# Kernel optimization log

Hardware: AMD Instinct MI355X
Metric: run time of the kernel (lower is better)

Reference implementation:

```python
import jax, jax.numpy as jnp
import numpy as np

N = 50000      # nodes
E = 800000     # edges
F_IN = 512     # num_features
H = 128        # hidden


def setup_inputs() -> dict:
    key = jax.random.key(0)
    ks = jax.random.split(key, 10)
    edge_index = jax.random.randint(ks[0], (2, E), 0, N, dtype=jnp.int64 if jax.config.jax_enable_x64 else jnp.int32)
    x = jax.random.normal(ks[1], (N, F_IN), jnp.float32)
    weights = jax.random.uniform(ks[2], (E,), jnp.float32)
    def w(i, shape, fan):
        return jax.random.normal(ks[i], shape, jnp.float32) / np.sqrt(fan).astype(np.float32)
    return {
        "edge_index": edge_index,
        "x": x,
        "weights": weights,
        "W_lin1": w(3, (F_IN, H), F_IN), "b_lin1": jnp.zeros((H,), jnp.float32),
        "W_conv1": w(4, (H, 2 * H), H), "b_conv1": jnp.zeros((2 * H,), jnp.float32),
        "W_mu": w(5, (2 * H, H), 2 * H), "b_mu": jnp.zeros((H,), jnp.float32),
        "W_lin": w(6, (2 * H, 1), 2 * H), "b_lin": jnp.zeros((1,), jnp.float32),
    }


def gcn_conv(x, W, b, src, dst, ew, n):
    """PyG GCNConv with edge weights: add self-loops (weight 1), symmetric norm, scatter-add."""
    loop = jnp.arange(n, dtype=src.dtype)
    s2 = jnp.concatenate([src, loop])
    d2 = jnp.concatenate([dst, loop])
    w2 = jnp.concatenate([ew, jnp.ones((n,), x.dtype)])
    deg = jax.ops.segment_sum(w2, d2, num_segments=n)          # weighted in-degree incl. self-loop
    dinv = jnp.where(deg > 0, deg, 1.0) ** -0.5
    dinv = jnp.where(deg > 0, dinv, 0.0)
    norm = dinv[s2] * w2 * dinv[d2]                            # [E+N]
    h = x @ W                                                   # [N, out]
    out = jax.ops.segment_sum(h[s2] * norm[:, None], d2, num_segments=n)
    return out + b


def reference(edge_index, x, weights, W_lin1, b_lin1, W_conv1, b_conv1, W_mu, b_mu, W_lin, b_lin):
    n = x.shape[0]
    src, dst = edge_index[0], edge_index[1]
    # eval mode: dropout is identity, VGAE.encode returns mu
    h = x @ W_lin1 + b_lin1                                     # lin1
    h = jax.nn.relu(gcn_conv(h, W_conv1, b_conv1, src, dst, weights, n))
    z = gcn_conv(h, W_mu, b_mu, src, dst, weights, n)           # mu == embeddings
    emb_edges = jnp.concatenate([z[src], z[dst]], axis=1)       # [E, 2H]
    out = jax.nn.sigmoid(emb_edges @ W_lin + b_lin)
    return out.squeeze(-1)                                      # [E]
```

## Files before the change

kernel.cpp:

```cpp
#include <hip/hip_runtime.h>
#include <hip/hip_bf16.h>
#include <math.h>


#define NSL 256
#define RSH 8
#define RNG 256

typedef __attribute__((ext_vector_type(8))) short bf16x8;
typedef __attribute__((ext_vector_type(4))) float f32x4;

static __device__ __forceinline__ ushort f2b(float f) {
    __hip_bfloat16 h = __float2bfloat16(f);
    return *(ushort*)&h;
}
static __device__ __forceinline__ float b2f(ushort u) {
    unsigned int v = ((unsigned int)u) << 16;
    return *(float*)&v;
}


__global__ __launch_bounds__(256) void bucket_count(const int* __restrict__ dst,
                                                    int* __restrict__ cntA, int E, int NR) {
    __shared__ int lc[256];
    const int b = blockIdx.x, t = threadIdx.x;
    lc[t] = 0;
    __syncthreads();
    const int beg = (int)((long long)b * E / NSL);
    const int end = (int)((long long)(b + 1) * E / NSL);
    for (int e = beg + t; e < end; e += 256) atomicAdd(&lc[dst[e] >> RSH], 1);
    __syncthreads();
    if (t < NR) cntA[b * NR + t] = lc[t];
}

__global__ __launch_bounds__(256) void range_scan(int* __restrict__ cntA,
                                                  int* __restrict__ rtot, int NR) {
    __shared__ int s_[256];
    const int r = blockIdx.x, t = threadIdx.x;
    int v = cntA[t * NR + r];
    s_[t] = v;
    __syncthreads();
    for (int off = 1; off < 256; off <<= 1) {
        int add = (t >= off) ? s_[t - off] : 0;
        __syncthreads();
        s_[t] += add;
        __syncthreads();
    }
    cntA[t * NR + r] = s_[t] - v;
    if (t == 255) rtot[r] = s_[t];
}

__global__ __launch_bounds__(256) void base_scan(const int* __restrict__ rtot,
                                                 int* __restrict__ baseOut, int NR) {
    __shared__ int s_[256];
    const int t = threadIdx.x;
    int v = (t < NR) ? rtot[t] : 0;
    s_[t] = v;
    __syncthreads();
    for (int off = 1; off < 256; off <<= 1) {
        int add = (t >= off) ? s_[t - off] : 0;
        __syncthreads();
        s_[t] += add;
        __syncthreads();
    }
    if (t < NR) baseOut[t] = s_[t] - v;
    if (t == NR - 1) baseOut[NR] = s_[t];
}

__global__ __launch_bounds__(256) void bucket_scatter(const int* __restrict__ src,
                                                      const int* __restrict__ dst,
                                                      const float* __restrict__ w,
                                                      const int* __restrict__ cntA,
                                                      const int* __restrict__ baseOut,
                                                      unsigned int* __restrict__ packB,
                                                      float* __restrict__ wB, int E, int NR) {
    __shared__ int cur[256];
    const int b = blockIdx.x, t = threadIdx.x;
    if (t < NR) cur[t] = cntA[b * NR + t] + baseOut[t];
    __syncthreads();
    const int beg = (int)((long long)b * E / NSL);
    const int end = (int)((long long)(b + 1) * E / NSL);
    for (int e = beg + t; e < end; e += 256) {
        int d = dst[e];
        int r = d >> RSH;
        int pos = atomicAdd(&cur[r], 1);
        packB[pos] = ((unsigned int)(d & (RNG - 1)) << 24) | (unsigned int)src[e];
        wB[pos] = w[e];
    }
}

__global__ __launch_bounds__(256) void range_deg(const unsigned int* __restrict__ packB,
                                                 const float* __restrict__ wB,
                                                 const int* __restrict__ baseOut,
                                                 float* __restrict__ dinv,
                                                 int* __restrict__ offs,
                                                 int N, int E) {
    __shared__ float lw[256];
    __shared__ int lc[256];
    __shared__ int sc[256];
    const int r = blockIdx.x, t = threadIdx.x;
    lw[t] = 0.f; lc[t] = 0;
    __syncthreads();
    const int beg = baseOut[r], end = baseOut[r + 1];
    for (int e = beg + t; e < end; e += 256) {
        unsigned int pk = packB[e];
        int dl = pk >> 24;
        atomicAdd(&lc[dl], 1);
        atomicAdd(&lw[dl], wB[e]);
    }
    __syncthreads();
    int v = lc[t];
    sc[t] = v;
    __syncthreads();
    for (int off = 1; off < 256; off <<= 1) {
        int add = (t >= off) ? sc[t - off] : 0;
        __syncthreads();
        sc[t] += add;
        __syncthreads();
    }
    int node = (r << RSH) + t;
    if (node < N) {
        dinv[node] = 1.0f / sqrtf(1.0f + lw[t]);
        offs[node] = beg + sc[t] - v;
    }
    if (r == 0 && t == 0) offs[N] = E;
}

__global__ __launch_bounds__(256) void csr_build(const unsigned int* __restrict__ packB,
                                                 const float* __restrict__ wB,
                                                 const int* __restrict__ baseOut,
                                                 const float* __restrict__ dinv,
                                                 const int* __restrict__ offs,
                                                 int* __restrict__ es,
                                                 float* __restrict__ en, int N) {
    __shared__ int cur[256];
    __shared__ float ldv[256];
    const int r = blockIdx.x, t = threadIdx.x;
    const int node = (r << RSH) + t;
    cur[t] = (node < N) ? offs[node] : 0;
    ldv[t] = (node < N) ? dinv[node] : 0.f;
    __syncthreads();
    const int beg = baseOut[r], end = baseOut[r + 1];
    for (int e = beg + t; e < end; e += 256) {
        unsigned int pk = packB[e];
        int dl = pk >> 24;
        int s = pk & 0xFFFFFF;
        float nrm = dinv[s] * wB[e] * ldv[dl];
        int pos = atomicAdd(&cur[dl], 1);
        es[pos] = s;
        en[pos] = nrm;
    }
}


__global__ __launch_bounds__(256) void tconv_kernel(const float* __restrict__ B,
                                                    ushort* __restrict__ BT, int K, int Nn) {
    int i = blockIdx.x * 256 + threadIdx.x;
    if (i < K * Nn) {
        int k = i / Nn, n = i % Nn;
        BT[(size_t)n * K + k] = f2b(B[i]);
    }
}

__global__ __launch_bounds__(256) void fold_kernel(const float* __restrict__ Wm,
                                                   const float* __restrict__ Wl,
                                                   const float* __restrict__ bm,
                                                   float* __restrict__ wmp,
                                                   float* __restrict__ wmq,
                                                   float* __restrict__ bpq) {
    int j = threadIdx.x;
    float sp = 0.f, sq = 0.f;
    for (int k = 0; k < 128; ++k) {
        float v = Wm[(size_t)j * 128 + k];
        sp += v * Wl[k];
        sq += v * Wl[128 + k];
    }
    wmp[j] = sp; wmq[j] = sq;
    if (j == 0) { float s = 0.f; for (int k = 0; k < 128; ++k) s += bm[k] * Wl[k];       bpq[0] = s; }
    if (j == 1) { float s = 0.f; for (int k = 0; k < 128; ++k) s += bm[k] * Wl[128 + k]; bpq[1] = s; }
}

__global__ __launch_bounds__(256) void gemm1_mfma(const float* __restrict__ A,
                                                  const ushort* __restrict__ BT,
                                                  const float* __restrict__ bias,
                                                  ushort* __restrict__ C, int M) {
    __shared__ ushort As[64 * 64];
    __shared__ ushort Bs[128 * 64];
    const int t = threadIdx.x;
    const int bm = blockIdx.x * 64;
    const int lane = t & 63;
    const int wid = t >> 6;
    const int wm = (wid >> 1) * 32, wn = (wid & 1) * 64;

    f32x4 acc[2][4] = {};

    const int arow0 = wid * 16 + (lane >> 4);
    const int acol  = (lane & 15) * 4;
    const int brow0 = wid * 32 + (lane >> 3);
    const int bcol  = (lane & 7) * 8;

    float4 aReg[4];
    uint4  bReg[4];

    auto issue = [&](int k0) {
#pragma unroll
        for (int j = 0; j < 4; ++j) {
            int row = arow0 + j * 4;
            bool valid = (bm + row) < M;
            aReg[j] = valid ? *(const float4*)(A + (size_t)(bm + row) * 512 + k0 + acol)
                            : make_float4(0.f, 0.f, 0.f, 0.f);
        }
#pragma unroll
        for (int j = 0; j < 4; ++j) {
            int row = brow0 + j * 8;
            bReg[j] = *(const uint4*)(BT + (size_t)row * 512 + k0 + bcol);
        }
    };

    issue(0);

#pragma unroll 1
    for (int tt = 0; tt < 8; ++tt) {
#pragma unroll
        for (int j = 0; j < 4; ++j) {
            int row = arow0 + j * 4;
            ushort4 u;
            u.x = f2b(aReg[j].x); u.y = f2b(aReg[j].y); u.z = f2b(aReg[j].z); u.w = f2b(aReg[j].w);
            int byte = (row * 128 + acol * 2) ^ ((row & 7) << 4);
            *(ushort4*)((char*)As + byte) = u;
        }
#pragma unroll
        for (int j = 0; j < 4; ++j) {
            int row = brow0 + j * 8;
            int byte = (row * 128 + bcol * 2) ^ ((row & 7) << 4);
            *(uint4*)((char*)Bs + byte) = bReg[j];
        }
        if (tt < 7) issue((tt + 1) * 64);
        __syncthreads();
#pragma unroll
        for (int ks = 0; ks < 2; ++ks) {
            bf16x8 af[2], bfr[4];
#pragma unroll
            for (int mi = 0; mi < 2; ++mi) {
                int row = wm + mi * 16 + (lane & 15);
                int byte = (row * 128 + ks * 64 + (lane >> 4) * 16) ^ ((row & 7) << 4);
                af[mi] = *(bf16x8*)((char*)As + byte);
            }
#pragma unroll
            for (int ni = 0; ni < 4; ++ni) {
                int row = wn + ni * 16 + (lane & 15);
                int byte = (row * 128 + ks * 64 + (lane >> 4) * 16) ^ ((row & 7) << 4);
                bfr[ni] = *(bf16x8*)((char*)Bs + byte);
            }
#pragma unroll
            for (int mi = 0; mi < 2; ++mi)
#pragma unroll
                for (int ni = 0; ni < 4; ++ni)
                    acc[mi][ni] = __builtin_amdgcn_mfma_f32_16x16x32_bf16(af[mi], bfr[ni], acc[mi][ni], 0, 0, 0);
        }
        __syncthreads();
    }
#pragma unroll
    for (int ni = 0; ni < 4; ++ni) {
        int col = wn + ni * 16 + (lane & 15);
        float bv = bias[col];
#pragma unroll
        for (int mi = 0; mi < 2; ++mi)
#pragma unroll
            for (int r = 0; r < 4; ++r) {
                int row = bm + wm + mi * 16 + (lane >> 4) * 4 + r;
                if (row < M) C[(size_t)row * 128 + col] = f2b(acc[mi][ni][r] + bv);
            }
    }
}

__global__ __launch_bounds__(256) void aggregate_bf16(const ushort* __restrict__ h,
                                                      const int* __restrict__ offs,
                                                      const int* __restrict__ es,
                                                      const float* __restrict__ en,
                                                      const float* __restrict__ dinv,
                                                      ushort* __restrict__ out, int n) {
    int wave = (int)((blockIdx.x * (size_t)blockDim.x + threadIdx.x) >> 6);
    int lane = threadIdx.x & 63;
    if (wave >= n) return;
    float di = dinv[wave];
    float sw = di * di;
    unsigned int hv = *(const unsigned int*)(h + (size_t)wave * 128 + lane * 2);
    float ax = sw * b2f((ushort)(hv & 0xffff));
    float ay = sw * b2f((ushort)(hv >> 16));
    int beg = offs[wave], end = offs[wave + 1];
    for (int e = beg; e < end; e += 8) {
        int sx[8]; float wx[8];
#pragma unroll
        for (int j = 0; j < 8; ++j) {
            bool v = (e + j) < end;
            sx[j] = v ? es[e + j] : wave;
            wx[j] = v ? en[e + j] : 0.f;
        }
        unsigned int vv[8];
#pragma unroll
        for (int j = 0; j < 8; ++j)
            vv[j] = *(const unsigned int*)(h + (size_t)sx[j] * 128 + lane * 2);
#pragma unroll
        for (int j = 0; j < 8; ++j) {
            ax += wx[j] * b2f((ushort)(vv[j] & 0xffff));
            ay += wx[j] * b2f((ushort)(vv[j] >> 16));
        }
    }
    unsigned int o = (unsigned int)f2b(ax) | ((unsigned int)f2b(ay) << 16);
    *(unsigned int*)(out + (size_t)wave * 128 + lane * 2) = o;
}

__global__ __launch_bounds__(512) void gemm2_pq(const ushort* __restrict__ A,
                                                const ushort* __restrict__ BT,
                                                const float* __restrict__ bc,
                                                const float* __restrict__ wmp,
                                                const float* __restrict__ wmq,
                                                float* __restrict__ pe,
                                                float* __restrict__ qe, int M) {
    __shared__ ushort As[64 * 64];
    __shared__ ushort Bs[256 * 64];
    __shared__ float partp[4][64];
    __shared__ float partq[4][64];
    const int t = threadIdx.x;
    const int bm = blockIdx.x * 64;
    const int lane = t & 63;
    const int wid = t >> 6;
    const int wm = (wid >> 2) * 32, wn = (wid & 3) * 64;

    f32x4 acc[2][4] = {};

    const int arow = t >> 3;
    const int acol = (t & 7) * 8;
    const int brow0 = wid * 32 + (lane >> 3);
    const int bcol  = (lane & 7) * 8;

    uint4 aReg;
    uint4 bReg[4];

    auto issue = [&](int k0) {
        bool valid = (bm + arow) < M;
        aReg = valid ? *(const uint4*)(A + (size_t)(bm + arow) * 128 + k0 + acol)
                     : make_uint4(0, 0, 0, 0);
#pragma unroll
        for (int j = 0; j < 4; ++j) {
            int row = brow0 + j * 8;
            bReg[j] = *(const uint4*)(BT + (size_t)row * 128 + k0 + bcol);
        }
    };

    issue(0);

#pragma unroll 1
    for (int tt = 0; tt < 2; ++tt) {
        {
            int byte = (arow * 128 + acol * 2) ^ ((arow & 7) << 4);
            *(uint4*)((char*)As + byte) = aReg;
        }
#pragma unroll
        for (int j = 0; j < 4; ++j) {
            int row = brow0 + j * 8;
            int byte = (row * 128 + bcol * 2) ^ ((row & 7) << 4);
            *(uint4*)((char*)Bs + byte) = bReg[j];
        }
        if (tt < 1) issue(64);
        __syncthreads();
#pragma unroll
        for (int ks = 0; ks < 2; ++ks) {
            bf16x8 af[2], bfr[4];
#pragma unroll
            for (int mi = 0; mi < 2; ++mi) {
                int row = wm + mi * 16 + (lane & 15);
                int byte = (row * 128 + ks * 64 + (lane >> 4) * 16) ^ ((row & 7) << 4);
                af[mi] = *(bf16x8*)((char*)As + byte);
            }
#pragma unroll
            for (int ni = 0; ni < 4; ++ni) {
                int row = wn + ni * 16 + (lane & 15);
                int byte = (row * 128 + ks * 64 + (lane >> 4) * 16) ^ ((row & 7) << 4);
                bfr[ni] = *(bf16x8*)((char*)Bs + byte);
            }
#pragma unroll
            for (int mi = 0; mi < 2; ++mi)
#pragma unroll
                for (int ni = 0; ni < 4; ++ni)
                    acc[mi][ni] = __builtin_amdgcn_mfma_f32_16x16x32_bf16(af[mi], bfr[ni], acc[mi][ni], 0, 0, 0);
        }
        __syncthreads();
    }

    float bcv[4], wpv[4], wqv[4];
#pragma unroll
    for (int ni = 0; ni < 4; ++ni) {
        int col = wn + ni * 16 + (lane & 15);
        bcv[ni] = bc[col];
        wpv[ni] = wmp[col];
        wqv[ni] = wmq[col];
    }
#pragma unroll
    for (int mi = 0; mi < 2; ++mi) {
#pragma unroll
        for (int r = 0; r < 4; ++r) {
            float sp = 0.f, sq = 0.f;
#pragma unroll
            for (int ni = 0; ni < 4; ++ni) {
                float h = fmaxf(acc[mi][ni][r] + bcv[ni], 0.f);
                sp += h * wpv[ni];
                sq += h * wqv[ni];
            }
#pragma unroll
            for (int off = 1; off < 16; off <<= 1) {
                sp += __shfl_xor(sp, off);
                sq += __shfl_xor(sq, off);
            }
            if ((lane & 15) == 0) {
                int row = wm + mi * 16 + (lane >> 4) * 4 + r;
                partp[wid & 3][row] = sp;
                partq[wid & 3][row] = sq;
            }
        }
    }
    __syncthreads();
    if (t < 64) {
        int row = t;
        if (bm + row < M)
            pe[bm + row] = partp[0][row] + partp[1][row] + partp[2][row] + partp[3][row];
    } else if (t < 128) {
        int row = t - 64;
        if (bm + row < M)
            qe[bm + row] = partq[0][row] + partq[1][row] + partq[2][row] + partq[3][row];
    }
}

__global__ __launch_bounds__(256) void agg_scalar(const float* __restrict__ pe,
                                                  const float* __restrict__ qe,
                                                  const int* __restrict__ offs,
                                                  const int* __restrict__ es,
                                                  const float* __restrict__ en,
                                                  const float* __restrict__ dinv,
                                                  const float* __restrict__ bpq,
                                                  float* __restrict__ p,
                                                  float* __restrict__ q, int n) {
    int i = blockIdx.x * 256 + threadIdx.x;
    if (i >= n) return;
    float di = dinv[i];
    float sw = di * di;
    float ap = sw * pe[i], aq = sw * qe[i];
    int beg = offs[i], end = offs[i + 1];
    for (int k = beg; k < end; k += 4) {
        int sx[4]; float wx[4];
#pragma unroll
        for (int j = 0; j < 4; ++j) {
            bool v = (k + j) < end;
            sx[j] = v ? es[k + j] : i;
            wx[j] = v ? en[k + j] : 0.f;
        }
        float pv[4], qv[4];
#pragma unroll
        for (int j = 0; j < 4; ++j) { pv[j] = pe[sx[j]]; qv[j] = qe[sx[j]]; }
#pragma unroll
        for (int j = 0; j < 4; ++j) { ap += wx[j] * pv[j]; aq += wx[j] * qv[j]; }
    }
    p[i] = ap + bpq[0];
    q[i] = aq + bpq[1];
}

__global__ __launch_bounds__(256) void edge_out_kernel(const int* __restrict__ src,
                                                       const int* __restrict__ dst,
                                                       const float* __restrict__ p,
                                                       const float* __restrict__ q,
                                                       const float* __restrict__ bl,
                                                       float* __restrict__ out, int e) {
    int i = blockIdx.x * 256 + threadIdx.x;
    if (i < e) {
        float t = p[src[i]] + q[dst[i]] + bl[0];
        out[i] = 1.0f / (1.0f + expf(-t));
    }
}


extern "C" void kernel_launch(void* const* d_in, const int* in_sizes, int n_in,
                              void* d_out, int out_size, void* d_ws, size_t ws_size,
                              hipStream_t stream) {
    const int*   edge_index = (const int*)d_in[0];
    const float* x   = (const float*)d_in[1];
    const float* w   = (const float*)d_in[2];
    const float* W1  = (const float*)d_in[3];
    const float* b1  = (const float*)d_in[4];
    const float* Wc  = (const float*)d_in[5];
    const float* bc  = (const float*)d_in[6];
    const float* Wm  = (const float*)d_in[7];
    const float* bm  = (const float*)d_in[8];
    const float* Wl  = (const float*)d_in[9];
    const float* bl  = (const float*)d_in[10];
    float* out = (float*)d_out;

    const int E  = in_sizes[2];
    const int H  = in_sizes[4];
    const int F  = in_sizes[3] / H;
    const int N  = in_sizes[1] / F;
    const int H2 = 2 * H;
    const int NR = (N + RNG - 1) / RNG;

    const int* src = edge_index;
    const int* dst = edge_index + E;

    char* ws = (char*)d_ws;
    size_t off = 0;
    auto alloc = [&](size_t bytes) -> void* {
        off = (off + 255) & ~(size_t)255;
        void* r = ws + off;
        off += bytes;
        return r;
    };
    int*          cntA    = (int*)         alloc((size_t)NSL * NR * 4);
    int*          rtot    = (int*)         alloc((size_t)NR * 4);
    int*          baseOut = (int*)         alloc((size_t)(NR + 1) * 4);
    unsigned int* packB   = (unsigned int*)alloc((size_t)E * 4);
    float*        wB      = (float*)       alloc((size_t)E * 4);
    float*        dinv    = (float*)       alloc((size_t)N * 4);
    int*          offs    = (int*)         alloc((size_t)(N + 1) * 4);
    int*          es      = (int*)         alloc((size_t)E * 4);
    float*        en      = (float*)       alloc((size_t)E * 4);
    ushort*       h0_bf   = (ushort*)      alloc((size_t)N * H * 2);
    ushort*       agg1_bf = (ushort*)      alloc((size_t)N * H * 2);
    ushort*       W1T     = (ushort*)      alloc((size_t)H * F * 2);
    ushort*       WcT     = (ushort*)      alloc((size_t)H2 * H * 2);
    float*        wmp     = (float*)       alloc(H2 * 4);
    float*        wmq     = (float*)       alloc(H2 * 4);
    float*        bpq     = (float*)       alloc(2 * 4);
    float*        pe      = (float*)       alloc((size_t)N * 4);
    float*        qe      = (float*)       alloc((size_t)N * 4);
    float*        p       = (float*)       alloc((size_t)N * 4);
    float*        q       = (float*)       alloc((size_t)N * 4);
    (void)ws_size; (void)n_in; (void)out_size;

    int nbN  = (N + 255) / 256;
    int nbE  = (E + 255) / 256;
    int nbW  = (int)(((size_t)N * 64 + 255) / 256);
    int nbM64 = (N + 63) / 64;

    bucket_count<<<NSL, 256, 0, stream>>>(dst, cntA, E, NR);
    range_scan<<<NR, 256, 0, stream>>>(cntA, rtot, NR);
    base_scan<<<1, 256, 0, stream>>>(rtot, baseOut, NR);
    bucket_scatter<<<NSL, 256, 0, stream>>>(src, dst, w, cntA, baseOut, packB, wB, E, NR);
    range_deg<<<NR, 256, 0, stream>>>(packB, wB, baseOut, dinv, offs, N, E);
    csr_build<<<NR, 256, 0, stream>>>(packB, wB, baseOut, dinv, offs, es, en, N);

    tconv_kernel<<<(F * H + 255) / 256, 256, 0, stream>>>(W1, W1T, F, H);
    tconv_kernel<<<(H * H2 + 255) / 256, 256, 0, stream>>>(Wc, WcT, H, H2);
    fold_kernel<<<1, 256, 0, stream>>>(Wm, Wl, bm, wmp, wmq, bpq);

    gemm1_mfma<<<nbM64, 256, 0, stream>>>(x, W1T, b1, h0_bf, N);
    aggregate_bf16<<<nbW, 256, 0, stream>>>(h0_bf, offs, es, en, dinv, agg1_bf, N);
    gemm2_pq<<<nbM64, 512, 0, stream>>>(agg1_bf, WcT, bc, wmp, wmq, pe, qe, N);
    agg_scalar<<<nbN, 256, 0, stream>>>(pe, qe, offs, es, en, dinv, bpq, p, q, N);
    edge_out_kernel<<<nbE, 256, 0, stream>>>(src, dst, p, q, bl, out, E);
}
```

Before: 197.1 us.

## Replace LDS-tiled GEMMs with direct-from-global register-fed MFMA kernels

Both dense GEMMs (lin1 and conv1 with the fused p/q projection) drop shared-memory staging and barriers. Each wave now loads its A fragments and B fragments straight from global memory into MFMA operand layout and covers all output columns, so the cross-wave partial-sum reduction through LDS in gemm2 goes away. The intent is to remove LDS traffic and sync overhead and rely on the caches for B reuse. In exchange, each wave issues many more uncoalesced global loads of the weight matrix, and register pressure rises from the larger accumulator arrays (up to 32 f32x4 in gemm2).

After: 198.2 us. Within noise of the previous version (+0.6%).

```diff
diff --git a/kernel.cpp b/kernel.cpp
--- a/kernel.cpp
+++ b/kernel.cpp
@@ -17,6 +17,12 @@
 static __device__ __forceinline__ float b2f(ushort u) {
     unsigned int v = ((unsigned int)u) << 16;
     return *(float*)&v;
+}
+static __device__ __forceinline__ bf16x8 cvt8(float4 a, float4 b) {
+    bf16x8 r;
+    r[0] = (short)f2b(a.x); r[1] = (short)f2b(a.y); r[2] = (short)f2b(a.z); r[3] = (short)f2b(a.w);
+    r[4] = (short)f2b(b.x); r[5] = (short)f2b(b.y); r[6] = (short)f2b(b.z); r[7] = (short)f2b(b.w);
+    return r;
 }
 
 
@@ -180,95 +186,52 @@
     if (j == 1) { float s = 0.f; for (int k = 0; k < 128; ++k) s += bm[k] * Wl[128 + k]; bpq[1] = s; }
 }
 
-__global__ __launch_bounds__(256) void gemm1_mfma(const float* __restrict__ A,
-                                                  const ushort* __restrict__ BT,
-                                                  const float* __restrict__ bias,
-                                                  ushort* __restrict__ C, int M) {
-    __shared__ ushort As[64 * 64];
-    __shared__ ushort Bs[128 * 64];
+__global__ __launch_bounds__(128) void gemm1_stream(const float* __restrict__ A,
+                                                    const ushort* __restrict__ BT,
+                                                    const float* __restrict__ bias,
+                                                    ushort* __restrict__ C, int M) {
     const int t = threadIdx.x;
-    const int bm = blockIdx.x * 64;
     const int lane = t & 63;
     const int wid = t >> 6;
-    const int wm = (wid >> 1) * 32, wn = (wid & 1) * 64;
-
-    f32x4 acc[2][4] = {};
-
-    const int arow0 = wid * 16 + (lane >> 4);
-    const int acol  = (lane & 15) * 4;
-    const int brow0 = wid * 32 + (lane >> 3);
-    const int bcol  = (lane & 7) * 8;
-
-    float4 aReg[4];
-    uint4  bReg[4];
-
-    auto issue = [&](int k0) {
-#pragma unroll
-        for (int j = 0; j < 4; ++j) {
-            int row = arow0 + j * 4;
-            bool valid = (bm + row) < M;
-            aReg[j] = valid ? *(const float4*)(A + (size_t)(bm + row) * 512 + k0 + acol)
-                            : make_float4(0.f, 0.f, 0.f, 0.f);
-        }
-#pragma unroll
-        for (int j = 0; j < 4; ++j) {
-            int row = brow0 + j * 8;
-            bReg[j] = *(const uint4*)(BT + (size_t)row * 512 + k0 + bcol);
-        }
-    };
-
-    issue(0);
-
-#pragma unroll 1
-    for (int tt = 0; tt < 8; ++tt) {
-#pragma unroll
-        for (int j = 0; j < 4; ++j) {
-            int row = arow0 + j * 4;
-            ushort4 u;
-            u.x = f2b(aReg[j].x); u.y = f2b(aReg[j].y); u.z = f2b(aReg[j].z); u.w = f2b(aReg[j].w);
-            int byte = (row * 128 + acol * 2) ^ ((row & 7) << 4);
-            *(ushort4*)((char*)As + byte) = u;
-        }
-#pragma unroll
-        for (int j = 0; j < 4; ++j) {
-            int row = brow0 + j * 8;
-            int byte = (row * 128 + bcol * 2) ^ ((row & 7) << 4);
-            *(uint4*)((char*)Bs + byte) = bReg[j];
-        }
-        if (tt < 7) issue((tt + 1) * 64);
-        __syncthreads();
-#pragma unroll
-        for (int ks = 0; ks < 2; ++ks) {
-            bf16x8 af[2], bfr[4];
-#pragma unroll
-            for (int mi = 0; mi < 2; ++mi) {
-                int row = wm + mi * 16 + (lane & 15);
-                int byte = (row * 128 + ks * 64 + (lane >> 4) * 16) ^ ((row & 7) << 4);
-                af[mi] = *(bf16x8*)((char*)As + byte);
-            }
-#pragma unroll
-            for (int ni = 0; ni < 4; ++ni) {
-                int row = wn + ni * 16 + (lane & 15);
-                int byte = (row * 128 + ks * 64 + (lane >> 4) * 16) ^ ((row & 7) << 4);
-                bfr[ni] = *(bf16x8*)((char*)Bs + byte);
-            }
-#pragma unroll
-            for (int mi = 0; mi < 2; ++mi)
-#pragma unroll
-                for (int ni = 0; ni < 4; ++ni)
-                    acc[mi][ni] = __builtin_amdgcn_mfma_f32_16x16x32_bf16(af[mi], bfr[ni], acc[mi][ni], 0, 0, 0);
-        }
-        __syncthreads();
-    }
-#pragma unroll
-    for (int ni = 0; ni < 4; ++ni) {
-        int col = wn + ni * 16 + (lane & 15);
+    const int r0 = blockIdx.x * 64 + wid * 32;
+    const int lrow = lane & 15;
+    const int lk   = (lane >> 4) * 8;
+
+    f32x4 acc[2][8] = {};
+
+    const float* a0 = A + (size_t)min(r0 + lrow,      M - 1) * 512 + lk;
+    const float* a1 = A + (size_t)min(r0 + 16 + lrow, M - 1) * 512 + lk;
+    const ushort* bp = BT + (size_t)lrow * 512 + lk;
+
+#pragma unroll 2
+    for (int ks = 0; ks < 16; ++ks) {
+        const int k0 = ks * 32;
+        float4 a0a = *(const float4*)(a0 + k0);
+        float4 a0b = *(const float4*)(a0 + k0 + 4);
+        float4 a1a = *(const float4*)(a1 + k0);
+        float4 a1b = *(const float4*)(a1 + k0 + 4);
+        bf16x8 bfr[8];
+#pragma unroll
+        for (int ni = 0; ni < 8; ++ni)
+            bfr[ni] = *(const bf16x8*)(bp + (size_t)ni * 16 * 512 + k0);
+        bf16x8 af0 = cvt8(a0a, a0b);
+        bf16x8 af1 = cvt8(a1a, a1b);
+#pragma unroll
+        for (int ni = 0; ni < 8; ++ni) {
+            acc[0][ni] = __builtin_amdgcn_mfma_f32_16x16x32_bf16(af0, bfr[ni], acc[0][ni], 0, 0, 0);
+            acc[1][ni] = __builtin_amdgcn_mfma_f32_16x16x32_bf16(af1, bfr[ni], acc[1][ni], 0, 0, 0);
+        }
+    }
+
+#pragma unroll
+    for (int ni = 0; ni < 8; ++ni) {
+        int col = ni * 16 + lrow;
         float bv = bias[col];
 #pragma unroll
         for (int mi = 0; mi < 2; ++mi)
 #pragma unroll
             for (int r = 0; r < 4; ++r) {
-                int row = bm + wm + mi * 16 + (lane >> 4) * 4 + r;
+                int row = r0 + mi * 16 + (lane >> 4) * 4 + r;
                 if (row < M) C[(size_t)row * 128 + col] = f2b(acc[mi][ni][r] + bv);
             }
     }
@@ -311,88 +274,43 @@
     *(unsigned int*)(out + (size_t)wave * 128 + lane * 2) = o;
 }
 
-__global__ __launch_bounds__(512) void gemm2_pq(const ushort* __restrict__ A,
-                                                const ushort* __restrict__ BT,
-                                                const float* __restrict__ bc,
-                                                const float* __restrict__ wmp,
-                                                const float* __restrict__ wmq,
-                                                float* __restrict__ pe,
-                                                float* __restrict__ qe, int M) {
-    __shared__ ushort As[64 * 64];
-    __shared__ ushort Bs[256 * 64];
-    __shared__ float partp[4][64];
-    __shared__ float partq[4][64];
+__global__ __launch_bounds__(128) void gemm2_stream(const ushort* __restrict__ A,
+                                                    const ushort* __restrict__ BT,
+                                                    const float* __restrict__ bc,
+                                                    const float* __restrict__ wmp,
+                                                    const float* __restrict__ wmq,
+                                                    float* __restrict__ pe,
+                                                    float* __restrict__ qe, int M) {
     const int t = threadIdx.x;
-    const int bm = blockIdx.x * 64;
     const int lane = t & 63;
     const int wid = t >> 6;
-    const int wm = (wid >> 2) * 32, wn = (wid & 3) * 64;
-
-    f32x4 acc[2][4] = {};
-
-    const int arow = t >> 3;
-    const int acol = (t & 7) * 8;
-    const int brow0 = wid * 32 + (lane >> 3);
-    const int bcol  = (lane & 7) * 8;
-
-    uint4 aReg;
-    uint4 bReg[4];
-
-    auto issue = [&](int k0) {
-        bool valid = (bm + arow) < M;
-        aReg = valid ? *(const uint4*)(A + (size_t)(bm + arow) * 128 + k0 + acol)
-                     : make_uint4(0, 0, 0, 0);
-#pragma unroll
-        for (int j = 0; j < 4; ++j) {
-            int row = brow0 + j * 8;
-            bReg[j] = *(const uint4*)(BT + (size_t)row * 128 + k0 + bcol);
-        }
-    };
-
-    issue(0);
-
-#pragma unroll 1
-    for (int tt = 0; tt < 2; ++tt) {
-        {
-            int byte = (arow * 128 + acol * 2) ^ ((arow & 7) << 4);
-            *(uint4*)((char*)As + byte) = aReg;
-        }
-#pragma unroll
-        for (int j = 0; j < 4; ++j) {
-            int row = brow0 + j * 8;
-            int byte = (row * 128 + bcol * 2) ^ ((row & 7) << 4);
-            *(uint4*)((char*)Bs + byte) = bReg[j];
-        }
-        if (tt < 1) issue(64);
-        __syncthreads();
-#pragma unroll
-        for (int ks = 0; ks < 2; ++ks) {
-            bf16x8 af[2], bfr[4];
-#pragma unroll
-            for (int mi = 0; mi < 2; ++mi) {
-                int row = wm + mi * 16 + (lane & 15);
-                int byte = (row * 128 + ks * 64 + (lane >> 4) * 16) ^ ((row & 7) << 4);
-                af[mi] = *(bf16x8*)((char*)As + byte);
-            }
-#pragma unroll
-            for (int ni = 0; ni < 4; ++ni) {
-                int row = wn + ni * 16 + (lane & 15);
-                int byte = (row * 128 + ks * 64 + (lane >> 4) * 16) ^ ((row & 7) << 4);
-                bfr[ni] = *(bf16x8*)((char*)Bs + byte);
-            }
-#pragma unroll
-            for (int mi = 0; mi < 2; ++mi)
-#pragma unroll
-                for (int ni = 0; ni < 4; ++ni)
-                    acc[mi][ni] = __builtin_amdgcn_mfma_f32_16x16x32_bf16(af[mi], bfr[ni], acc[mi][ni], 0, 0, 0);
-        }
-        __syncthreads();
-    }
-
-    float bcv[4], wpv[4], wqv[4];
-#pragma unroll
-    for (int ni = 0; ni < 4; ++ni) {
-        int col = wn + ni * 16 + (lane & 15);
+    const int r0 = blockIdx.x * 64 + wid * 32;
+    const int lrow = lane & 15;
+    const int lk   = (lane >> 4) * 8;
+
+    f32x4 acc[2][16] = {};
+
+    const ushort* a0 = A + (size_t)min(r0 + lrow,      M - 1) * 128 + lk;
+    const ushort* a1 = A + (size_t)min(r0 + 16 + lrow, M - 1) * 128 + lk;
+    const ushort* bp = BT + (size_t)lrow * 128 + lk;
+
+#pragma unroll
+    for (int ks = 0; ks < 4; ++ks) {
+        const int k0 = ks * 32;
+        bf16x8 af0 = *(const bf16x8*)(a0 + k0);
+        bf16x8 af1 = *(const bf16x8*)(a1 + k0);
+#pragma unroll
+        for (int ni = 0; ni < 16; ++ni) {
+            bf16x8 bfr = *(const bf16x8*)(bp + (size_t)ni * 16 * 128 + k0);
+            acc[0][ni] = __builtin_amdgcn_mfma_f32_16x16x32_bf16(af0, bfr, acc[0][ni], 0, 0, 0);
+            acc[1][ni] = __builtin_amdgcn_mfma_f32_16x16x32_bf16(af1, bfr, acc[1][ni], 0, 0, 0);
+        }
+    }
+
+    float bcv[16], wpv[16], wqv[16];
+#pragma unroll
+    for (int ni = 0; ni < 16; ++ni) {
+        int col = ni * 16 + lrow;
         bcv[ni] = bc[col];
         wpv[ni] = wmp[col];
         wqv[ni] = wmq[col];
@@ -403,7 +321,7 @@
         for (int r = 0; r < 4; ++r) {
             float sp = 0.f, sq = 0.f;
 #pragma unroll
-            for (int ni = 0; ni < 4; ++ni) {
+            for (int ni = 0; ni < 16; ++ni) {
                 float h = fmaxf(acc[mi][ni][r] + bcv[ni], 0.f);
                 sp += h * wpv[ni];
                 sq += h * wqv[ni];
@@ -413,22 +331,11 @@
                 sp += __shfl_xor(sp, off);
                 sq += __shfl_xor(sq, off);
             }
-            if ((lane & 15) == 0) {
-                int row = wm + mi * 16 + (lane >> 4) * 4 + r;
-                partp[wid & 3][row] = sp;
-                partq[wid & 3][row] = sq;
+            if (lrow == 0) {
+                int row = r0 + mi * 16 + (lane >> 4) * 4 + r;
+                if (row < M) { pe[row] = sp; qe[row] = sq; }
             }
         }
-    }
-    __syncthreads();
-    if (t < 64) {
-        int row = t;
-        if (bm + row < M)
-            pe[bm + row] = partp[0][row] + partp[1][row] + partp[2][row] + partp[3][row];
-    } else if (t < 128) {
-        int row = t - 64;
-        if (bm + row < M)
-            qe[bm + row] = partq[0][row] + partq[1][row] + partq[2][row] + partq[3][row];
     }
 }
 
@@ -535,10 +442,10 @@
     float*        q       = (float*)       alloc((size_t)N * 4);
     (void)ws_size; (void)n_in; (void)out_size;
 
-    int nbN  = (N + 255) / 256;
-    int nbE  = (E + 255) / 256;
-    int nbW  = (int)(((size_t)N * 64 + 255) / 256);
-    int nbM64 = (N + 63) / 64;
+    int nbN   = (N + 255) / 256;
+    int nbE   = (E + 255) / 256;
+    int nbW   = (int)(((size_t)N * 64 + 255) / 256);
+    int nbS   = (N + 63) / 64;
 
     bucket_count<<<NSL, 256, 0, stream>>>(dst, cntA, E, NR);
     range_scan<<<NR, 256, 0, stream>>>(cntA, rtot, NR);
@@ -551,9 +458,9 @@
     tconv_kernel<<<(H * H2 + 255) / 256, 256, 0, stream>>>(Wc, WcT, H, H2);
     fold_kernel<<<1, 256, 0, stream>>>(Wm, Wl, bm, wmp, wmq, bpq);
 
-    gemm1_mfma<<<nbM64, 256, 0, stream>>>(x, W1T, b1, h0_bf, N);
+    gemm1_stream<<<nbS, 128, 0, stream>>>(x, W1T, b1, h0_bf, N);
     aggregate_bf16<<<nbW, 256, 0, stream>>>(h0_bf, offs, es, en, dinv, agg1_bf, N);
-    gemm2_pq<<<nbM64, 512, 0, stream>>>(agg1_bf, WcT, bc, wmp, wmq, pe, qe, N);
+    gemm2_stream<<<nbS, 128, 0, stream>>>(agg1_bf, WcT, bc, wmp, wmq, pe, qe, N);
     agg_scalar<<<nbN, 256, 0, stream>>>(pe, qe, offs, es, en, dinv, bpq, p, q, N);
     edge_out_kernel<<<nbE, 256, 0, stream>>>(src, dst, p, q, bl, out, E);
 }
```
